# Kernel optimization log

Hardware: AMD Instinct MI355X
Metric: run time of the kernel (lower is better)

The kernel has to match this reference:

```python
import jax, jax.numpy as jnp
import numpy as np

RADIUS = 2
TEMP = 1.0
B, CIN, D, H, W = 1, 32, 64, 64, 64
PROJ, OUT = 64, 64
K = (2 * RADIUS + 1) ** 3  # 125 local offsets

_OFFSETS = np.array([(dz, dy, dx)
                     for dz in range(-RADIUS, RADIUS + 1)
                     for dy in range(-RADIUS, RADIUS + 1)
                     for dx in range(-RADIUS, RADIUS + 1)], dtype=np.int32)


def _conv3d(x, w, b, pad):
    y = jax.lax.conv_general_dilated(
        x, w, window_strides=(1, 1, 1), padding=[(pad, pad)] * 3,
        dimension_numbers=('NCDHW', 'OIDHW', 'NCDHW'))
    if b is not None:
        y = y + b[None, :, None, None, None]
    return y


def _l2norm(x):
    # torch F.normalize(dim=1): x / max(||x||_2, 1e-12)
    n = jnp.sqrt(jnp.sum(x * x, axis=1, keepdims=True))
    return x / jnp.maximum(n, 1e-12)


def _inorm(x, eps=1e-5):
    # InstanceNorm3d (affine=False): normalize over spatial dims per (B,C)
    mu = jnp.mean(x, axis=(2, 3, 4), keepdims=True)
    var = jnp.mean((x - mu) ** 2, axis=(2, 3, 4), keepdims=True)
    return (x - mu) * jax.lax.rsqrt(var + eps)


def _ntn(x):
    return jnp.nan_to_num(x, nan=0.0, posinf=0.0, neginf=0.0)


def setup_inputs() -> dict:
    key = jax.random.key(0)
    ks = jax.random.split(key, 8)
    s = 0.05
    return {
        'source_features': jax.random.normal(ks[0], (B, CIN, D, H, W), jnp.float32),
        'warped_target_features': jax.random.normal(ks[1], (B, CIN, D, H, W), jnp.float32),
        'w_src': jax.random.normal(ks[2], (PROJ, CIN, 1, 1, 1), jnp.float32) * s,
        'b_src': jnp.zeros((PROJ,), jnp.float32),
        'w_tgt': jax.random.normal(ks[3], (PROJ, CIN, 1, 1, 1), jnp.float32) * s,
        'b_tgt': jnp.zeros((PROJ,), jnp.float32),
        'w_enc1': jax.random.normal(ks[4], (OUT, K + 5, 3, 3, 3), jnp.float32) * s,
        'b_enc1': jnp.zeros((OUT,), jnp.float32),
        'w_enc2': jax.random.normal(ks[5], (OUT, OUT, 3, 3, 3), jnp.float32) * s,
        'b_enc2': jnp.zeros((OUT,), jnp.float32),
    }


def reference(source_features, warped_target_features, w_src, b_src, w_tgt, b_tgt,
              w_enc1, b_enc1, w_enc2, b_enc2):
    sp = _l2norm(_conv3d(source_features, w_src, b_src, 0))      # [B,P,D,H,W]
    tp = _l2norm(_conv3d(warped_target_features, w_tgt, b_tgt, 0))
    pt = jnp.pad(tp, ((0, 0), (0, 0), (RADIUS, RADIUS), (RADIUS, RADIUS), (RADIUS, RADIUS)),
                 mode='edge')  # replicate pad

    starts = jnp.asarray(_OFFSETS + RADIUS, jnp.int32)  # [K,3] slice starts

    def corr_one(st):
        sh = jax.lax.dynamic_slice(pt, (0, 0, st[0], st[1], st[2]), (B, PROJ, D, H, W))
        return jnp.sum(sp * sh, axis=1)  # [B,D,H,W]

    corr = jnp.transpose(jax.vmap(corr_one)(starts), (1, 0, 2, 3, 4))  # [B,K,D,H,W]
    scaled = corr / max(TEMP, 1e-6)

    top2 = jax.lax.top_k(jnp.moveaxis(scaled, 1, -1), 2)[0]  # [B,D,H,W,2]
    m = jnp.moveaxis(top2[..., 0:1], -1, 1)   # running max   [B,1,D,H,W]
    s2 = jnp.moveaxis(top2[..., 1:2], -1, 1)  # second max

    p = jnp.exp(scaled - m)                    # [B,K,D,H,W]
    Z = jnp.sum(p, axis=1, keepdims=True)
    inv = 1.0 / jnp.maximum(Z, 1e-8)

    offv = jnp.asarray(_OFFSETS, jnp.float32)  # [K,3]
    expected_offset = _ntn(jnp.einsum('bkdhw,kc->bcdhw', p, offv) * inv)
    confidence = _ntn(jnp.minimum(inv, 1.0))   # max-prob = exp(m-m)/Z
    second_prob = jnp.exp(s2 - m) * inv
    margin = _ntn(jnp.maximum(confidence - second_prob, 0.0))
    entropy = _ntn(m + jnp.log(jnp.maximum(Z, 1e-8))
                   - jnp.sum(p * scaled, axis=1, keepdims=True) * inv)

    enc_in = jnp.concatenate([corr, expected_offset, confidence, entropy], axis=1)  # [B,K+5,D,H,W]
    h = _conv3d(enc_in, w_enc1, b_enc1, 1)
    h = jax.nn.gelu(_inorm(h), approximate=False)
    h = _conv3d(h, w_enc2, b_enc2, 1)
    h = jax.nn.gelu(_inorm(h), approximate=False)
    encoded_features = _ntn(h)

    return expected_offset, confidence, margin, entropy, encoded_features
```

## Files before the change

### kernel.cpp

```cpp
#include <hip/hip_runtime.h>

#define DEV __device__ __forceinline__

typedef short bf16x8 __attribute__((ext_vector_type(8)));
typedef float f32x4 __attribute__((ext_vector_type(4)));

static const int NVOX = 262144;

DEV float bflo(unsigned int u) { return __uint_as_float(u << 16); }
DEV float bfhi(unsigned int u) { return __uint_as_float(u & 0xffff0000u); }
DEV float bf2f(unsigned short s) { return __uint_as_float(((unsigned int)s) << 16); }
DEV unsigned short f2bf(float f) {
    unsigned int x = __float_as_uint(f);
    x += 0x7fffu + ((x >> 16) & 1u);
    return (unsigned short)(x >> 16);
}
DEV float ldin(const void* p, int i, int f) {
    return f ? ((const float*)p)[i] : bf2f(((const unsigned short*)p)[i]);
}

__global__ void sniff_kernel(const unsigned short* __restrict__ src, int* __restrict__ flag) {
    __shared__ int cnt[256];
    int t = threadIdx.x;
    int c = 0;
    for (int i = t; i < 4096; i += 256) {
        unsigned int u = (unsigned int)src[i] & 0x7fffu;
        c += (u >= 0x4900u) ? 1 : 0;
    }
    cnt[t] = c;
    __syncthreads();
    for (int s = 128; s > 0; s >>= 1) {
        if (t < s) cnt[t] += cnt[t + s];
        __syncthreads();
    }
    if (t == 0) *flag = (cnt[0] > 8) ? 1 : 0;
}

__global__ void prep_kernel(const void* __restrict__ w1, const void* __restrict__ w2,
                            const void* __restrict__ bsv, const void* __restrict__ btv,
                            const void* __restrict__ b1v, const void* __restrict__ b2v,
                            const int* __restrict__ flag,
                            unsigned short* __restrict__ Wf1,
                            unsigned short* __restrict__ Wf2,
                            float* __restrict__ fbias) {
    const int f = *flag;
    int idx = blockIdx.x * 256 + threadIdx.x;
    const int N1  = 27 * 4 * 4 * 512;
    const int N1E = 2 * 4 * 512;
    const int N2  = 27 * 2 * 4 * 512;
    if (idx < N1) {
        int frag = idx >> 9;
        int r    = idx & 511;
        int lane = r >> 3, j = r & 7;
        int nt = frag & 3;
        int tk = frag >> 2;
        int tap = tk >> 2, kc = tk & 3;
        int o  = nt * 16 + (lane & 15);
        int cp = kc * 32 + (lane >> 4) * 8 + j;
        Wf1[idx] = f2bf(ldin(w1, (o * 130 + cp) * 27 + tap, f));
    } else if (idx < N1 + N1E) {
        int i2 = idx - N1;
        int frag = i2 >> 9;
        int r    = i2 & 511;
        int lane = r >> 3, j = r & 7;
        int nt = frag & 3, kc = frag >> 2;
        int o   = nt * 16 + (lane & 15);
        int kap = kc * 32 + (lane >> 4) * 8 + j;
        unsigned short val = 0;
        if (kap < 54) {
            int tap = kap >> 1, ch = 128 + (kap & 1);
            val = f2bf(ldin(w1, (o * 130 + ch) * 27 + tap, f));
        }
        Wf1[idx] = val;
    } else if (idx < N1 + N1E + N2) {
        int i2 = idx - N1 - N1E;
        int frag = i2 >> 9;
        int r    = i2 & 511;
        int lane = r >> 3, j = r & 7;
        int nt = frag & 3;
        int tk = frag >> 2;
        int tap = tk >> 1, kc = tk & 1;
        int o = nt * 16 + (lane & 15);
        int c = kc * 32 + (lane >> 4) * 8 + j;
        Wf2[i2] = f2bf(ldin(w2, (o * 64 + c) * 27 + tap, f));
    } else if (idx < N1 + N1E + N2 + 256) {
        int j = idx - N1 - N1E - N2;
        const void* bp = (j < 64) ? bsv : (j < 128) ? btv : (j < 192) ? b1v : b2v;
        fbias[j] = ldin(bp, j & 63, f);
    }
}

__global__ __launch_bounds__(256) void proj_kernel(
        const void* __restrict__ Xsrc, const void* __restrict__ Xtgt,
        const void* __restrict__ Wsrc, const void* __restrict__ Wtgt,
        const float* __restrict__ fbias, const int* __restrict__ flag,
        unsigned short* __restrict__ SP, unsigned short* __restrict__ TP) {
    const int f = *flag;
    const void* Xin = blockIdx.y ? Xtgt : Xsrc;
    const void* W   = blockIdx.y ? Wtgt : Wsrc;
    const float* Bb = fbias + (blockIdx.y ? 64 : 0);
    unsigned short* Outp = blockIdx.y ? TP : SP;

    __shared__ float ws[2048];
    const int t = threadIdx.x;
    for (int i = t; i < 2048; i += 256) {
        int ci = i >> 6, o = i & 63;
        ws[i] = ldin(W, o * 32 + ci, f);
    }
    __syncthreads();

    const size_t v = (size_t)blockIdx.x * 256 + t;
    float acc[64];
#pragma unroll
    for (int o = 0; o < 64; ++o) acc[o] = Bb[o];
    if (f) {
        const float* Xf = (const float*)Xin;
        for (int ci = 0; ci < 32; ++ci) {
            float x = Xf[(size_t)ci * NVOX + v];
            const float4* wr = (const float4*)(ws + ci * 64);
#pragma unroll
            for (int o4 = 0; o4 < 16; ++o4) {
                float4 w4 = wr[o4];
                acc[o4 * 4 + 0] = fmaf(w4.x, x, acc[o4 * 4 + 0]);
                acc[o4 * 4 + 1] = fmaf(w4.y, x, acc[o4 * 4 + 1]);
                acc[o4 * 4 + 2] = fmaf(w4.z, x, acc[o4 * 4 + 2]);
                acc[o4 * 4 + 3] = fmaf(w4.w, x, acc[o4 * 4 + 3]);
            }
        }
    } else {
        const unsigned short* Xb = (const unsigned short*)Xin;
        for (int ci = 0; ci < 32; ++ci) {
            float x = bf2f(Xb[(size_t)ci * NVOX + v]);
            const float4* wr = (const float4*)(ws + ci * 64);
#pragma unroll
            for (int o4 = 0; o4 < 16; ++o4) {
                float4 w4 = wr[o4];
                acc[o4 * 4 + 0] = fmaf(w4.x, x, acc[o4 * 4 + 0]);
                acc[o4 * 4 + 1] = fmaf(w4.y, x, acc[o4 * 4 + 1]);
                acc[o4 * 4 + 2] = fmaf(w4.z, x, acc[o4 * 4 + 2]);
                acc[o4 * 4 + 3] = fmaf(w4.w, x, acc[o4 * 4 + 3]);
            }
        }
    }
    float s = 0.f;
#pragma unroll
    for (int o = 0; o < 64; ++o) s = fmaf(acc[o], acc[o], s);
    float scale = 1.f / fmaxf(sqrtf(s), 1e-12f);

    unsigned int pk[32];
#pragma unroll
    for (int o = 0; o < 32; ++o)
        pk[o] = (unsigned int)f2bf(acc[2 * o] * scale) |
                ((unsigned int)f2bf(acc[2 * o + 1] * scale) << 16);
    uint4* outp = (uint4*)(Outp + v * 64);
#pragma unroll
    for (int j = 0; j < 8; ++j)
        outp[j] = make_uint4(pk[4 * j], pk[4 * j + 1], pk[4 * j + 2], pk[4 * j + 3]);
}

DEV void tp_load(const unsigned short* __restrict__ TP, int t, int z, int y,
                 int it, uint4* pre) {
    const int zc = min(max(z + it / 5 - 2, 0), 63);
    const int yc = min(max(y + it % 5 - 2, 0), 63);
    const unsigned short* tbase = TP + ((size_t)zc * 64 + yc) * 4096;
#pragma unroll
    for (int j = 0; j < 3; ++j) {
        int i = t + j * 256;
        uint4 vv = make_uint4(0u, 0u, 0u, 0u);
        if (i < 640) {
            int pp = i >> 3, cc = i & 7;
            int xc = min(max(pp - 2, 0), 63);
            vv = *(const uint4*)(tbase + xc * 64 + cc * 8);
        }
        pre[j] = vv;
    }
}

DEV void tp_commit(unsigned short* buf, int t, const uint4* pre) {
#pragma unroll
    for (int j = 0; j < 3; ++j) {
        int i = t + j * 256;
        if (i < 640) {
            int pp = i >> 3, cc = i & 7;
            *(uint4*)((char*)buf + pp * 128 + ((cc ^ (pp & 7)) * 16)) = pre[j];
        }
    }
}

__global__ __launch_bounds__(256) void corr_kernel(
        const unsigned short* __restrict__ SP, const unsigned short* __restrict__ TP,
        unsigned short* __restrict__ X1, float* __restrict__ Out) {
    __shared__ __align__(16) unsigned short spb[64 * 64];
    __shared__ __align__(16) unsigned short tpb[2][80 * 64];
    __shared__ __align__(16) unsigned short stage[64 * 128];

    const int t = threadIdx.x;
    const int wv = t >> 6, lane = t & 63;
    const int q = lane >> 4, l16 = lane & 15;
    const int x0 = wv * 16;

    const int bid = blockIdx.x;
    const int wg = (bid & 7) * 512 + (bid >> 3);
    const int z = wg >> 6, y = wg & 63;
    const size_t vbase = ((size_t)z * 64 + y) * 64;

    {
        int i0 = t, i1 = t + 256;
        uint4 spv0 = *(const uint4*)(SP + (vbase + (i0 >> 3)) * 64 + (i0 & 7) * 8);
        uint4 spv1 = *(const uint4*)(SP + (vbase + (i1 >> 3)) * 64 + (i1 & 7) * 8);
        int xa = i0 >> 3, ca = i0 & 7;
        int xb = i1 >> 3, cb = i1 & 7;
        *(uint4*)((char*)spb + xa * 128 + ((ca ^ (xa & 7)) * 16)) = spv0;
        *(uint4*)((char*)spb + xb * 128 + ((cb ^ (xb & 7)) * 16)) = spv1;
    }

    uint4 pre[3];
    tp_load(TP, t, z, y, 0, pre);
    int p = 0;
    for (int it = 0; it < 25; ++it) {
        tp_commit(tpb[p], t, pre);
        __syncthreads();
        if (it < 24) tp_load(TP, t, z, y, it + 1, pre);

        f32x4 acc[2] = {{0.f, 0.f, 0.f, 0.f}, {0.f, 0.f, 0.f, 0.f}};
        {
            const char* sb = (const char*)spb;
            const char* tb = (const char*)tpb[p];
            const int xr = x0 + l16;
#pragma unroll
            for (int kc = 0; kc < 2; ++kc) {
                bf16x8 a = *(const bf16x8*)(sb + xr * 128 + (((kc * 4 + q) ^ (xr & 7)) * 16));
#pragma unroll
                for (int nt = 0; nt < 2; ++nt) {
                    const int pr = x0 + nt * 16 + l16;
                    bf16x8 b = *(const bf16x8*)(tb + pr * 128 + (((kc * 4 + q) ^ (pr & 7)) * 16));
                    acc[nt] = __builtin_amdgcn_mfma_f32_16x16x32_bf16(a, b, acc[nt], 0, 0, 0);
                }
            }
        }
        const int kb = it * 5;
        char* sg = (char*)stage;
#pragma unroll
        for (int nt = 0; nt < 2; ++nt) {
#pragma unroll
            for (int r = 0; r < 4; ++r) {
                int ml = q * 4 + r;
                int dxp = nt * 16 + l16 - ml;
                if ((unsigned)dxp < 5u) {
                    int xl = x0 + ml;
                    *(unsigned short*)(sg + xl * 256 + (((kb + dxp) * 2) ^ ((xl & 7) << 4))) =
                        f2bf(acc[nt][r]);
                }
            }
        }
        p ^= 1;
    }

    __syncthreads();
    {
        const int vox = t >> 2, part = t & 3;
        const int sx = (vox & 7) << 4;
        const char* sg = (const char*)stage;
        uint4 u[4];
#pragma unroll
        for (int j = 0; j < 4; ++j)
            u[j] = *(const uint4*)(sg + vox * 256 + ((part * 64 + j * 16) ^ sx));

        float m = -1e30f, s2 = -1e30f;
#pragma unroll
        for (int j = 0; j < 4; ++j) {
            const unsigned int uu[4] = {u[j].x, u[j].y, u[j].z, u[j].w};
#pragma unroll
            for (int w = 0; w < 4; ++w) {
                int k = part * 32 + j * 8 + w * 2;
                float d0 = (k < 125) ? bflo(uu[w]) : -1e30f;
                float d1 = (k + 1 < 125) ? bfhi(uu[w]) : -1e30f;
                float lo0 = fminf(d0, m); m = fmaxf(d0, m); s2 = fmaxf(s2, lo0);
                float lo1 = fminf(d1, m); m = fmaxf(d1, m); s2 = fmaxf(s2, lo1);
            }
        }
#pragma unroll
        for (int off = 1; off <= 2; off <<= 1) {
            float om = __shfl_xor(m, off, 64);
            float os = __shfl_xor(s2, off, 64);
            float lo = fminf(m, om);
            m = fmaxf(m, om);
            s2 = fmaxf(fmaxf(s2, os), lo);
        }
        int kk = part * 32;
        int dz0 = kk / 25, rem = kk - dz0 * 25, dy0 = rem / 5, dx0 = rem - dy0 * 5;
        float fx = (float)(dx0 - 2), fy = (float)(dy0 - 2), fz = (float)(dz0 - 2);
        float Zs = 0.f, S1 = 0.f, Ox = 0.f, Oy = 0.f, Oz = 0.f;
#pragma unroll
        for (int j = 0; j < 4; ++j) {
            const unsigned int uu[4] = {u[j].x, u[j].y, u[j].z, u[j].w};
#pragma unroll
            for (int w = 0; w < 8; ++w) {
                int k = part * 32 + j * 8 + w;
                bool ok = (k < 125);
                float d = (w & 1) ? bfhi(uu[w >> 1]) : bflo(uu[w >> 1]);
                d = ok ? d : 0.f;
                float e = ok ? __expf(d - m) : 0.f;
                Zs += e; S1 = fmaf(e, d, S1);
                Ox = fmaf(e, fx, Ox); Oy = fmaf(e, fy, Oy); Oz = fmaf(e, fz, Oz);
                fx += 1.f;
                if (fx > 2.5f) { fx = -2.f; fy += 1.f; if (fy > 2.5f) { fy = -2.f; fz += 1.f; } }
            }
        }
#pragma unroll
        for (int off = 1; off <= 2; off <<= 1) {
            Zs += __shfl_xor(Zs, off, 64);
            S1 += __shfl_xor(S1, off, 64);
            Ox += __shfl_xor(Ox, off, 64);
            Oy += __shfl_xor(Oy, off, 64);
            Oz += __shfl_xor(Oz, off, 64);
        }
        if (part == 0) {
            float inv  = 1.f / fmaxf(Zs, 1e-8f);
            float eoz = Oz * inv, eoy = Oy * inv, eox = Ox * inv;
            float conf = fminf(inv, 1.f);
            float marg = fmaxf(conf - __expf(s2 - m) * inv, 0.f);
            float ent  = m + __logf(fmaxf(Zs, 1e-8f)) - S1 * inv;
            char* sgw = (char*)stage;
            *(unsigned short*)(sgw + vox * 256 + (250 ^ sx)) = f2bf(eoz);
            *(unsigned short*)(sgw + vox * 256 + (252 ^ sx)) = f2bf(eoy);
            *(unsigned short*)(sgw + vox * 256 + (254 ^ sx)) = f2bf(eox);
            const size_t v = vbase + vox;
            *(unsigned int*)(X1 + v * 160 + 128) =
                (unsigned int)f2bf(conf) | ((unsigned int)f2bf(ent) << 16);
            Out[v]                    = eoz;
            Out[(size_t)NVOX + v]     = eoy;
            Out[(size_t)2 * NVOX + v] = eox;
            Out[(size_t)3 * NVOX + v] = conf;
            Out[(size_t)4 * NVOX + v] = marg;
            Out[(size_t)5 * NVOX + v] = ent;
        }
    }
    __syncthreads();

#pragma unroll
    for (int j = 0; j < 4; ++j) {
        int i = t + j * 256;
        int vox = i >> 4, cc = i & 15;
        *(uint4*)(X1 + (vbase + vox) * 160 + (size_t)cc * 8) =
            *(const uint4*)((const char*)stage + vox * 256 + ((cc * 16) ^ ((vox & 7) << 4)));
    }
}

template <int XSTRIDE, int CPAD, int LSTRIDE, int KC, int NLD, bool TAIL>
__global__ __launch_bounds__(256) void conv3_kernel(
        const unsigned short* __restrict__ Xin, const unsigned short* __restrict__ Wf,
        const unsigned short* __restrict__ Wfe,
        const float* __restrict__ Bias, unsigned short* __restrict__ Out) {
    __shared__ unsigned short rowbuf[2][66 * LSTRIDE];
    const int lin = blockIdx.x;
    const int z = (lin & 7) * 8 + ((lin >> 3) >> 6);
    const int y = (lin >> 3) & 63;
    const int t = threadIdx.x;
    const int wv = t >> 6, lane = t & 63;
    const int quad = lane >> 4, l16 = lane & 15;
    const int mt2 = (wv & 1) * 2;
    const int nt2 = (wv >> 1) * 2;
    const int CH16 = CPAD / 8;

    f32x4 acc[2][2] = {{{0.f,0.f,0.f,0.f},{0.f,0.f,0.f,0.f}},
                       {{0.f,0.f,0.f,0.f},{0.f,0.f,0.f,0.f}}};

    uint4 pre[NLD];
    {
        const int zz = z - 1, yy = y - 1;
        const bool valid = (unsigned)zz < 64u && (unsigned)yy < 64u;
        const unsigned short* base = Xin + (((size_t)(valid ? zz : 0) * 64 + (valid ? yy : 0)) * 64) * XSTRIDE;
#pragma unroll
        for (int i = 0; i < NLD; ++i) {
            int idx = t + i * 256;
            uint4 val = make_uint4(0u, 0u, 0u, 0u);
            if (idx < 66 * CH16) {
                int xi = idx / CH16, ci = idx % CH16;
                int gx = xi - 1;
                if (valid && gx >= 0 && gx < 64) val = *(const uint4*)(base + gx * XSTRIDE + ci * 8);
            }
            pre[i] = val;
        }
    }

    if (TAIL) {
        unsigned short* ebuf = &rowbuf[1][0];
#pragma unroll
        for (int i2 = 0; i2 < 8; ++i2) {
            int i = t + i2 * 256;
            int vox = i >> 5, slot = i & 31;
            unsigned int val = 0u;
            int kap;
            if (slot < 27) {
                int dz = slot / 9 - 1, dy = (slot / 3) % 3 - 1, dxx = slot % 3 - 1;
                int zz = z + dz, yy = y + dy, xx = vox + dxx;
                kap = slot * 2;
                if ((unsigned)zz < 64u && (unsigned)yy < 64u && (unsigned)xx < 64u)
                    val = *(const unsigned int*)(Xin + (((size_t)zz * 64 + yy) * 64 + xx) * XSTRIDE + 128);
            } else {
                kap = 54 + (slot - 27) * 2;
            }
            *(unsigned int*)(ebuf + vox * 72 + kap) = val;
        }
        __syncthreads();
#pragma unroll
        for (int kc = 0; kc < 2; ++kc) {
            bf16x8 bte[2];
#pragma unroll
            for (int nl = 0; nl < 2; ++nl)
                bte[nl] = *(const bf16x8*)(Wfe + (size_t)(kc * 4 + nt2 + nl) * 512 + lane * 8);
#pragma unroll
            for (int ml = 0; ml < 2; ++ml) {
                bf16x8 a = *(const bf16x8*)(ebuf + ((mt2 + ml) * 16 + l16) * 72 + (kc * 4 + quad) * 8);
#pragma unroll
                for (int nl = 0; nl < 2; ++nl)
                    acc[ml][nl] = __builtin_amdgcn_mfma_f32_16x16x32_bf16(a, bte[nl], acc[ml][nl], 0, 0, 0);
            }
        }
        __syncthreads();
    }

    int p = 0;
    for (int it = 0; it < 9; ++it) {
#pragma unroll
        for (int i = 0; i < NLD; ++i) {
            int idx = t + i * 256;
            if (idx < 66 * CH16) {
                int xi = idx / CH16, ci = idx % CH16;
                *(uint4*)(&rowbuf[p][xi * LSTRIDE + ci * 8]) = pre[i];
            }
        }
        __syncthreads();
        if (it < 8) {
            const int itn = it + 1;
            const int zz = z + itn / 3 - 1, yy = y + itn % 3 - 1;
            const bool valid = (unsigned)zz < 64u && (unsigned)yy < 64u;
            const unsigned short* base = Xin + (((size_t)(valid ? zz : 0) * 64 + (valid ? yy : 0)) * 64) * XSTRIDE;
#pragma unroll
            for (int i = 0; i < NLD; ++i) {
                int idx = t + i * 256;
                uint4 val = make_uint4(0u, 0u, 0u, 0u);
                if (idx < 66 * CH16) {
                    int xi = idx / CH16, ci = idx % CH16;
                    int gx = xi - 1;
                    if (valid && gx >= 0 && gx < 64) val = *(const uint4*)(base + gx * XSTRIDE + ci * 8);
                }
                pre[i] = val;
            }
        }
        const unsigned short* rp = rowbuf[p];
#pragma unroll
        for (int dx = 0; dx < 3; ++dx) {
            const int tap = it * 3 + dx;
            const unsigned short* wt = Wf + ((size_t)tap * KC * 4) * 512 + lane * 8;
            bf16x8 bf[KC][2];
#pragma unroll
            for (int kc = 0; kc < KC; ++kc)
#pragma unroll
                for (int nl = 0; nl < 2; ++nl)
                    bf[kc][nl] = *(const bf16x8*)(wt + (size_t)(kc * 4 + nt2 + nl) * 512);
#pragma unroll
            for (int kc = 0; kc < KC; ++kc) {
#pragma unroll
                for (int ml = 0; ml < 2; ++ml) {
                    bf16x8 a = *(const bf16x8*)(&rp[((mt2 + ml) * 16 + l16 + dx) * LSTRIDE + kc * 32 + quad * 8]);
#pragma unroll
                    for (int nl = 0; nl < 2; ++nl)
                        acc[ml][nl] = __builtin_amdgcn_mfma_f32_16x16x32_bf16(a, bf[kc][nl], acc[ml][nl], 0, 0, 0);
                }
            }
        }
        p ^= 1;
    }

    const size_t vbase = ((size_t)z * 64 + y) * 64;
#pragma unroll
    for (int ml = 0; ml < 2; ++ml) {
#pragma unroll
        for (int nl = 0; nl < 2; ++nl) {
            const int oc = (nt2 + nl) * 16 + l16;
            const float bv = Bias[oc];
#pragma unroll
            for (int r = 0; r < 4; ++r)
                Out[(vbase + (mt2 + ml) * 16 + quad * 4 + r) * 64 + oc] = f2bf(acc[ml][nl][r] + bv);
        }
    }
}

__global__ __launch_bounds__(256) void stats_kernel(
        const unsigned short* __restrict__ H, float* __restrict__ stats) {
    const int t = threadIdx.x;
    const int c = t & 63, g = t >> 6;
    float s = 0.f, q = 0.f;
    for (int v = blockIdx.x * 4 + g; v < NVOX; v += gridDim.x * 4) {
        float x = bf2f(H[(size_t)v * 64 + c]);
        s += x; q = fmaf(x, x, q);
    }
    __shared__ float ls[256], lq[256];
    ls[t] = s; lq[t] = q;
    __syncthreads();
    if (t < 64) {
        s = ls[t] + ls[t + 64] + ls[t + 128] + ls[t + 192];
        q = lq[t] + lq[t + 64] + lq[t + 128] + lq[t + 192];
        atomicAdd(&stats[c], s);
        atomicAdd(&stats[64 + c], q);
    }
}

__global__ void finalize_kernel(const float* __restrict__ stats, float* __restrict__ musr) {
    int c = threadIdx.x;
    if (c < 64) {
        float mu  = stats[c] * (1.0f / 262144.0f);
        float var = stats[64 + c] * (1.0f / 262144.0f) - mu * mu;
        musr[c] = mu;
        musr[64 + c] = rsqrtf(var + 1e-5f);
    }
}

__global__ __launch_bounds__(256) void norm_gelu_kernel(
        const unsigned short* __restrict__ H, const float* __restrict__ musr,
        unsigned short* __restrict__ G) {
    const size_t base = ((size_t)blockIdx.x * 256 + threadIdx.x) * 8;
    uint4 u = *(const uint4*)(H + base);
    const int c0 = (int)(base & 63);
    const unsigned int uu[4] = {u.x, u.y, u.z, u.w};
    unsigned int w[4];
#pragma unroll
    for (int p = 0; p < 4; ++p) {
        int c = c0 + p * 2;
        float x0 = (bflo(uu[p]) - musr[c]) * musr[64 + c];
        float x1 = (bfhi(uu[p]) - musr[c + 1]) * musr[64 + c + 1];
        float g0 = 0.5f * x0 * (1.f + erff(x0 * 0.70710678118f));
        float g1 = 0.5f * x1 * (1.f + erff(x1 * 0.70710678118f));
        w[p] = (unsigned int)f2bf(g0) | ((unsigned int)f2bf(g1) << 16);
    }
    *(uint4*)(G + base) = make_uint4(w[0], w[1], w[2], w[3]);
}

__global__ __launch_bounds__(256) void out_final_kernel(
        const unsigned short* __restrict__ H2, const float* __restrict__ musr,
        float* __restrict__ OutEnc) {
    __shared__ float tile[64 * 260];
    const int t = threadIdx.x;
    const size_t v0 = (size_t)blockIdx.x * 256;
#pragma unroll
    for (int i = 0; i < 8; ++i) {
        int chunk = t + i * 256;
        uint4 u = *(const uint4*)(H2 + v0 * 64 + (size_t)chunk * 8);
        int vox = chunk >> 3;
        int c0 = (chunk & 7) * 8;
        const unsigned int uu[4] = {u.x, u.y, u.z, u.w};
#pragma unroll
        for (int p = 0; p < 4; ++p) {
            int c = c0 + p * 2;
            float x0 = (bflo(uu[p]) - musr[c]) * musr[64 + c];
            float x1 = (bfhi(uu[p]) - musr[c + 1]) * musr[64 + c + 1];
            tile[c * 260 + vox]       = 0.5f * x0 * (1.f + erff(x0 * 0.70710678118f));
            tile[(c + 1) * 260 + vox] = 0.5f * x1 * (1.f + erff(x1 * 0.70710678118f));
        }
    }
    __syncthreads();
    const int c = t >> 2, sub = t & 3;
#pragma unroll
    for (int iter = 0; iter < 16; ++iter) {
        int fq = iter * 4 + sub;
        float4 val = *(const float4*)(&tile[c * 260 + fq * 4]);
        *(float4*)(OutEnc + (size_t)c * NVOX + v0 + fq * 4) = val;
    }
}

extern "C" void kernel_launch(void* const* d_in, const int* in_sizes, int n_in,
                              void* d_out, int out_size, void* d_ws, size_t ws_size,
                              hipStream_t stream) {
    const void* src  = d_in[0];
    const void* tgt  = d_in[1];
    const void* wsrc = d_in[2];
    const void* bsrc = d_in[3];
    const void* wtgt = d_in[4];
    const void* btgt = d_in[5];
    const void* w1   = d_in[6];
    const void* b1   = d_in[7];
    const void* w2   = d_in[8];
    const void* b2   = d_in[9];
    float* out = (float*)d_out;

    char* ws = (char*)d_ws;
    unsigned short* TPb = (unsigned short*)(ws);
    unsigned short* SPb = (unsigned short*)(ws + 33554432);
    unsigned short* X1  = (unsigned short*)(ws + 67108864);
    unsigned short* Wf1 = (unsigned short*)(ws + 150994944);
    unsigned short* Wf2 = (unsigned short*)(ws + 151547904);
    int*   flag   = (int*)  (ws + 151769088);
    float* fbias  = (float*)(ws + 151769152);
    float* stats1 = (float*)(ws + 151770176);
    float* musr1  = (float*)(ws + 151770688);
    float* stats2 = (float*)(ws + 151771200);
    float* musr2  = (float*)(ws + 151771712);
    unsigned short* H1 = SPb;
    unsigned short* G1 = TPb;
    unsigned short* H2 = X1;
    unsigned short* Wf1e = Wf1 + 27 * 4 * 4 * 512;

    (void)hipMemsetAsync(stats1, 0, 2048, stream);
    sniff_kernel<<<1, 256, 0, stream>>>((const unsigned short*)src, flag);
    prep_kernel<<<1313, 256, 0, stream>>>(w1, w2, bsrc, btgt, b1, b2, flag, Wf1, Wf2, fbias);
    proj_kernel<<<dim3(1024, 2), 256, 0, stream>>>(src, tgt, wsrc, wtgt, fbias, flag, SPb, TPb);
    corr_kernel<<<4096, 256, 0, stream>>>(SPb, TPb, X1, out);
    conv3_kernel<160, 128, 136, 4, 5, true><<<4096, 256, 0, stream>>>(X1, Wf1, Wf1e, fbias + 128, H1);
    stats_kernel<<<256, 256, 0, stream>>>(H1, stats1);
    finalize_kernel<<<1, 64, 0, stream>>>(stats1, musr1);
    norm_gelu_kernel<<<8192, 256, 0, stream>>>(H1, musr1, G1);
    conv3_kernel<64, 64, 72, 2, 3, false><<<4096, 256, 0, stream>>>(G1, Wf2, nullptr, fbias + 192, H2);
    stats_kernel<<<256, 256, 0, stream>>>(H2, stats2);
    finalize_kernel<<<1, 64, 0, stream>>>(stats2, musr2);
    out_final_kernel<<<1024, 256, 0, stream>>>(H2, musr2, out + 6 * (size_t)NVOX);
}
```

Measured before the change: 736.0 us.

## Stage tiles via direct global-to-LDS loads with XOR swizzle in corr and conv3

Replaces the register-staged global loads followed by LDS stores with direct global_load_lds transfers in both the correlation and 3x3x3 conv kernels, using an XOR swizzle in place of padded LDS rows. The corr kernel now holds its source-projection A fragments in registers instead of LDS. The conv kernels skip out-of-range z/y neighbour rows entirely instead of loading zeros, write zero halo rows once, and add min-waves occupancy hints. The goal is to cut VGPR pressure and load/store instruction overhead while overlapping the next row's fetch with MFMA work; the risk is that the async LDS loads are waited on only by the existing barriers, and the halo and skip logic is subtle.

After: 758.0 us. 1.03x slower.

```diff
diff --git a/kernel.cpp b/kernel.cpp
--- a/kernel.cpp
+++ b/kernel.cpp
@@ -17,6 +17,12 @@
 }
 DEV float ldin(const void* p, int i, int f) {
     return f ? ((const float*)p)[i] : bf2f(((const unsigned short*)p)[i]);
+}
+
+DEV void gld16(const unsigned short* g, unsigned short* l) {
+    __builtin_amdgcn_global_load_lds(
+        (const __attribute__((address_space(1))) unsigned int*)g,
+        (__attribute__((address_space(3))) unsigned int*)l, 16, 0, 0);
 }
 
 __global__ void sniff_kernel(const unsigned short* __restrict__ src, int* __restrict__ flag) {
@@ -158,39 +164,9 @@
         outp[j] = make_uint4(pk[4 * j], pk[4 * j + 1], pk[4 * j + 2], pk[4 * j + 3]);
 }
 
-DEV void tp_load(const unsigned short* __restrict__ TP, int t, int z, int y,
-                 int it, uint4* pre) {
-    const int zc = min(max(z + it / 5 - 2, 0), 63);
-    const int yc = min(max(y + it % 5 - 2, 0), 63);
-    const unsigned short* tbase = TP + ((size_t)zc * 64 + yc) * 4096;
-#pragma unroll
-    for (int j = 0; j < 3; ++j) {
-        int i = t + j * 256;
-        uint4 vv = make_uint4(0u, 0u, 0u, 0u);
-        if (i < 640) {
-            int pp = i >> 3, cc = i & 7;
-            int xc = min(max(pp - 2, 0), 63);
-            vv = *(const uint4*)(tbase + xc * 64 + cc * 8);
-        }
-        pre[j] = vv;
-    }
-}
-
-DEV void tp_commit(unsigned short* buf, int t, const uint4* pre) {
-#pragma unroll
-    for (int j = 0; j < 3; ++j) {
-        int i = t + j * 256;
-        if (i < 640) {
-            int pp = i >> 3, cc = i & 7;
-            *(uint4*)((char*)buf + pp * 128 + ((cc ^ (pp & 7)) * 16)) = pre[j];
-        }
-    }
-}
-
 __global__ __launch_bounds__(256) void corr_kernel(
         const unsigned short* __restrict__ SP, const unsigned short* __restrict__ TP,
         unsigned short* __restrict__ X1, float* __restrict__ Out) {
-    __shared__ __align__(16) unsigned short spb[64 * 64];
     __shared__ __align__(16) unsigned short tpb[2][80 * 64];
     __shared__ __align__(16) unsigned short stage[64 * 128];
 
@@ -204,38 +180,48 @@
     const int z = wg >> 6, y = wg & 63;
     const size_t vbase = ((size_t)z * 64 + y) * 64;
 
-    {
-        int i0 = t, i1 = t + 256;
-        uint4 spv0 = *(const uint4*)(SP + (vbase + (i0 >> 3)) * 64 + (i0 & 7) * 8);
-        uint4 spv1 = *(const uint4*)(SP + (vbase + (i1 >> 3)) * 64 + (i1 & 7) * 8);
-        int xa = i0 >> 3, ca = i0 & 7;
-        int xb = i1 >> 3, cb = i1 & 7;
-        *(uint4*)((char*)spb + xa * 128 + ((ca ^ (xa & 7)) * 16)) = spv0;
-        *(uint4*)((char*)spb + xb * 128 + ((cb ^ (xb & 7)) * 16)) = spv1;
-    }
-
-    uint4 pre[3];
-    tp_load(TP, t, z, y, 0, pre);
+    const unsigned short* arow = SP + (vbase + x0 + l16) * 64 + q * 8;
+    const bf16x8 a0 = *(const bf16x8*)(arow);
+    const bf16x8 a1 = *(const bf16x8*)(arow + 32);
+
+    auto stage_tp = [&](int it, int b) {
+        const int zc = min(max(z + it / 5 - 2, 0), 63);
+        const int yc = min(max(y + it % 5 - 2, 0), 63);
+        const unsigned short* tb = TP + ((size_t)zc * 64 + yc) * 4096;
+#pragma unroll
+        for (int j = 0; j < 2; ++j) {
+            int c = t + j * 256;
+            int pp = c >> 3, cc = c & 7;
+            int xc = min(max(pp - 2, 0), 63);
+            gld16(tb + xc * 64 + ((cc ^ (pp & 7)) * 8),
+                  &tpb[b][(wv * 64 + j * 256) * 8]);
+        }
+        if (wv < 2) {
+            int c = 512 + wv * 64 + lane;
+            int pp = c >> 3, cc = c & 7;
+            int xc = min(max(pp - 2, 0), 63);
+            gld16(tb + xc * 64 + ((cc ^ (pp & 7)) * 8),
+                  &tpb[b][(512 + wv * 64) * 8]);
+        }
+    };
+
+    stage_tp(0, 0);
+    __syncthreads();
+
     int p = 0;
     for (int it = 0; it < 25; ++it) {
-        tp_commit(tpb[p], t, pre);
-        __syncthreads();
-        if (it < 24) tp_load(TP, t, z, y, it + 1, pre);
+        if (it < 24) stage_tp(it + 1, p ^ 1);
 
         f32x4 acc[2] = {{0.f, 0.f, 0.f, 0.f}, {0.f, 0.f, 0.f, 0.f}};
         {
-            const char* sb = (const char*)spb;
             const char* tb = (const char*)tpb[p];
-            const int xr = x0 + l16;
-#pragma unroll
-            for (int kc = 0; kc < 2; ++kc) {
-                bf16x8 a = *(const bf16x8*)(sb + xr * 128 + (((kc * 4 + q) ^ (xr & 7)) * 16));
-#pragma unroll
-                for (int nt = 0; nt < 2; ++nt) {
-                    const int pr = x0 + nt * 16 + l16;
-                    bf16x8 b = *(const bf16x8*)(tb + pr * 128 + (((kc * 4 + q) ^ (pr & 7)) * 16));
-                    acc[nt] = __builtin_amdgcn_mfma_f32_16x16x32_bf16(a, b, acc[nt], 0, 0, 0);
-                }
+#pragma unroll
+            for (int nt = 0; nt < 2; ++nt) {
+                const int pr = x0 + nt * 16 + l16;
+                bf16x8 b0 = *(const bf16x8*)(tb + pr * 128 + ((q ^ (pr & 7)) * 16));
+                bf16x8 b1 = *(const bf16x8*)(tb + pr * 128 + (((4 + q) ^ (pr & 7)) * 16));
+                acc[nt] = __builtin_amdgcn_mfma_f32_16x16x32_bf16(a0, b0, acc[nt], 0, 0, 0);
+                acc[nt] = __builtin_amdgcn_mfma_f32_16x16x32_bf16(a1, b1, acc[nt], 0, 0, 0);
             }
         }
         const int kb = it * 5;
@@ -253,10 +239,10 @@
                 }
             }
         }
+        __syncthreads();
         p ^= 1;
     }
 
-    __syncthreads();
     {
         const int vox = t >> 2, part = t & 3;
         const int sx = (vox & 7) << 4;
@@ -347,12 +333,12 @@
     }
 }
 
-template <int XSTRIDE, int CPAD, int LSTRIDE, int KC, int NLD, bool TAIL>
-__global__ __launch_bounds__(256) void conv3_kernel(
+template <int XSTRIDE, int CPAD, int KC, int NLD, int MINW, bool TAIL>
+__global__ __launch_bounds__(256, MINW) void conv3_kernel(
         const unsigned short* __restrict__ Xin, const unsigned short* __restrict__ Wf,
         const unsigned short* __restrict__ Wfe,
         const float* __restrict__ Bias, unsigned short* __restrict__ Out) {
-    __shared__ unsigned short rowbuf[2][66 * LSTRIDE];
+    __shared__ __align__(16) unsigned short rowbuf[2][66 * CPAD];
     const int lin = blockIdx.x;
     const int z = (lin & 7) * 8 + ((lin >> 3) >> 6);
     const int y = (lin >> 3) & 63;
@@ -366,22 +352,21 @@
     f32x4 acc[2][2] = {{{0.f,0.f,0.f,0.f},{0.f,0.f,0.f,0.f}},
                        {{0.f,0.f,0.f,0.f},{0.f,0.f,0.f,0.f}}};
 
-    uint4 pre[NLD];
+    auto stage_row = [&](int zz, int yy, int b) {
+        const unsigned short* base = Xin + (((size_t)zz * 64 + yy) * 64) * XSTRIDE;
+#pragma unroll
+        for (int i = 0; i < NLD; ++i) {
+            int chunk = wv * 64 + lane + i * 256;
+            int xi = chunk / CH16 + 1;
+            int cc = chunk % CH16;
+            gld16(base + (xi - 1) * XSTRIDE + ((cc ^ (xi & 7)) * 8),
+                  &rowbuf[b][CPAD + (size_t)(wv * 64 + i * 256) * 8]);
+        }
+    };
+
     {
         const int zz = z - 1, yy = y - 1;
-        const bool valid = (unsigned)zz < 64u && (unsigned)yy < 64u;
-        const unsigned short* base = Xin + (((size_t)(valid ? zz : 0) * 64 + (valid ? yy : 0)) * 64) * XSTRIDE;
-#pragma unroll
-        for (int i = 0; i < NLD; ++i) {
-            int idx = t + i * 256;
-            uint4 val = make_uint4(0u, 0u, 0u, 0u);
-            if (idx < 66 * CH16) {
-                int xi = idx / CH16, ci = idx % CH16;
-                int gx = xi - 1;
-                if (valid && gx >= 0 && gx < 64) val = *(const uint4*)(base + gx * XSTRIDE + ci * 8);
-            }
-            pre[i] = val;
-        }
+        if ((unsigned)zz < 64u && (unsigned)yy < 64u) stage_row(zz, yy, 0);
     }
 
     if (TAIL) {
@@ -421,56 +406,45 @@
         __syncthreads();
     }
 
+    if (t < 4 * CH16) {
+        int b = t / (2 * CH16), r2 = (t / CH16) & 1, c = t % CH16;
+        *(uint4*)(&rowbuf[b][(size_t)(r2 * 65) * CPAD + c * 8]) = make_uint4(0u, 0u, 0u, 0u);
+    }
+    __syncthreads();
+
     int p = 0;
     for (int it = 0; it < 9; ++it) {
-#pragma unroll
-        for (int i = 0; i < NLD; ++i) {
-            int idx = t + i * 256;
-            if (idx < 66 * CH16) {
-                int xi = idx / CH16, ci = idx % CH16;
-                *(uint4*)(&rowbuf[p][xi * LSTRIDE + ci * 8]) = pre[i];
+        if (it < 8) {
+            const int z2 = z + (it + 1) / 3 - 1, y2 = y + (it + 1) % 3 - 1;
+            if ((unsigned)z2 < 64u && (unsigned)y2 < 64u) stage_row(z2, y2, p ^ 1);
+        }
+        const int zz = z + it / 3 - 1, yy = y + it % 3 - 1;
+        if ((unsigned)zz < 64u && (unsigned)yy < 64u) {
+            const unsigned short* rp = rowbuf[p];
+#pragma unroll
+            for (int dx = 0; dx < 3; ++dx) {
+                const int tap = it * 3 + dx;
+                const unsigned short* wt = Wf + ((size_t)tap * KC * 4) * 512 + lane * 8;
+                bf16x8 bf[KC][2];
+#pragma unroll
+                for (int kc = 0; kc < KC; ++kc)
+#pragma unroll
+                    for (int nl = 0; nl < 2; ++nl)
+                        bf[kc][nl] = *(const bf16x8*)(wt + (size_t)(kc * 4 + nt2 + nl) * 512);
+#pragma unroll
+                for (int kc = 0; kc < KC; ++kc) {
+#pragma unroll
+                    for (int ml = 0; ml < 2; ++ml) {
+                        const int row = (mt2 + ml) * 16 + l16 + dx;
+                        bf16x8 a = *(const bf16x8*)(&rp[(size_t)row * CPAD + ((kc * 4 + quad) ^ (row & 7)) * 8]);
+#pragma unroll
+                        for (int nl = 0; nl < 2; ++nl)
+                            acc[ml][nl] = __builtin_amdgcn_mfma_f32_16x16x32_bf16(a, bf[kc][nl], acc[ml][nl], 0, 0, 0);
+                    }
+                }
             }
         }
         __syncthreads();
-        if (it < 8) {
-            const int itn = it + 1;
-            const int zz = z + itn / 3 - 1, yy = y + itn % 3 - 1;
-            const bool valid = (unsigned)zz < 64u && (unsigned)yy < 64u;
-            const unsigned short* base = Xin + (((size_t)(valid ? zz : 0) * 64 + (valid ? yy : 0)) * 64) * XSTRIDE;
-#pragma unroll
-            for (int i = 0; i < NLD; ++i) {
-                int idx = t + i * 256;
-                uint4 val = make_uint4(0u, 0u, 0u, 0u);
-                if (idx < 66 * CH16) {
-                    int xi = idx / CH16, ci = idx % CH16;
-                    int gx = xi - 1;
-                    if (valid && gx >= 0 && gx < 64) val = *(const uint4*)(base + gx * XSTRIDE + ci * 8);
-                }
-                pre[i] = val;
-            }
-        }
-        const unsigned short* rp = rowbuf[p];
-#pragma unroll
-        for (int dx = 0; dx < 3; ++dx) {
-            const int tap = it * 3 + dx;
-            const unsigned short* wt = Wf + ((size_t)tap * KC * 4) * 512 + lane * 8;
-            bf16x8 bf[KC][2];
-#pragma unroll
-            for (int kc = 0; kc < KC; ++kc)
-#pragma unroll
-                for (int nl = 0; nl < 2; ++nl)
-                    bf[kc][nl] = *(const bf16x8*)(wt + (size_t)(kc * 4 + nt2 + nl) * 512);
-#pragma unroll
-            for (int kc = 0; kc < KC; ++kc) {
-#pragma unroll
-                for (int ml = 0; ml < 2; ++ml) {
-                    bf16x8 a = *(const bf16x8*)(&rp[((mt2 + ml) * 16 + l16 + dx) * LSTRIDE + kc * 32 + quad * 8]);
-#pragma unroll
-                    for (int nl = 0; nl < 2; ++nl)
-                        acc[ml][nl] = __builtin_amdgcn_mfma_f32_16x16x32_bf16(a, bf[kc][nl], acc[ml][nl], 0, 0, 0);
-                }
-            }
-        }
         p ^= 1;
     }
 
@@ -607,11 +581,11 @@
     prep_kernel<<<1313, 256, 0, stream>>>(w1, w2, bsrc, btgt, b1, b2, flag, Wf1, Wf2, fbias);
     proj_kernel<<<dim3(1024, 2), 256, 0, stream>>>(src, tgt, wsrc, wtgt, fbias, flag, SPb, TPb);
     corr_kernel<<<4096, 256, 0, stream>>>(SPb, TPb, X1, out);
-    conv3_kernel<160, 128, 136, 4, 5, true><<<4096, 256, 0, stream>>>(X1, Wf1, Wf1e, fbias + 128, H1);
+    conv3_kernel<160, 128, 4, 4, 4, true><<<4096, 256, 0, stream>>>(X1, Wf1, Wf1e, fbias + 128, H1);
     stats_kernel<<<256, 256, 0, stream>>>(H1, stats1);
     finalize_kernel<<<1, 64, 0, stream>>>(stats1, musr1);
     norm_gelu_kernel<<<8192, 256, 0, stream>>>(H1, musr1, G1);
-    conv3_kernel<64, 64, 72, 2, 3, false><<<4096, 256, 0, stream>>>(G1, Wf2, nullptr, fbias + 192, H2);
+    conv3_kernel<64, 64, 2, 2, 6, false><<<4096, 256, 0, stream>>>(G1, Wf2, nullptr, fbias + 192, H2);
     stats_kernel<<<256, 256, 0, stream>>>(H2, stats2);
     finalize_kernel<<<1, 64, 0, stream>>>(stats2, musr2);
     out_final_kernel<<<1024, 256, 0, stream>>>(H2, musr2, out + 6 * (size_t)NVOX);
```
